# Performance work log

Measured on AMD Instinct MI355X. Metric: run time of the kernel, lower is better.

Reference implementation:

```python
import jax, jax.numpy as jnp
import numpy as np

N_NODES = 50000
N_EDGES = 800000
IN_CH = 128
HIDDEN = 32
HEADS = 4
NEG_SLOPE = 0.2


def segment_softmax(e, seg, num_segments):
    # numerically stable softmax over edges grouped by destination node
    m = jax.ops.segment_max(e, seg, num_segments=num_segments)
    ex = jnp.exp(e - m[seg])
    denom = jax.ops.segment_sum(ex, seg, num_segments=num_segments)
    return ex / denom[seg]


def gat_layer(x, src, dst, W, a_src, a_dst, b, num_nodes, concat):
    H, C = a_src.shape
    h = (x @ W).reshape(num_nodes, H, C)            # (N, H, C)
    alpha_s = jnp.einsum('nhc,hc->nh', h, a_src)    # (N, H)
    alpha_d = jnp.einsum('nhc,hc->nh', h, a_dst)    # (N, H)
    e = jax.nn.leaky_relu(alpha_s[src] + alpha_d[dst], negative_slope=NEG_SLOPE)  # (E, H)
    att = segment_softmax(e, dst, num_nodes)        # (E, H)
    out = jax.ops.segment_sum(h[src] * att[:, :, None], dst, num_segments=num_nodes)  # (N, H, C)
    if concat:
        out = out.reshape(num_nodes, H * C)
    else:
        out = out.mean(axis=1)
    return out + b


def setup_inputs() -> dict:
    key = jax.random.key(0)
    ks = jax.random.split(key, 12)
    s = 0.1
    return {
        'x': jax.random.normal(ks[0], (N_NODES, IN_CH), dtype=jnp.float32),
        'edge_index': jax.random.randint(ks[1], (2, N_EDGES), 0, N_NODES, dtype=jnp.int64),
        'W1': jax.random.normal(ks[2], (IN_CH, HEADS * HIDDEN), dtype=jnp.float32) * s,
        'a_src1': jax.random.normal(ks[3], (HEADS, HIDDEN), dtype=jnp.float32) * s,
        'a_dst1': jax.random.normal(ks[4], (HEADS, HIDDEN), dtype=jnp.float32) * s,
        'b1': jnp.zeros((HEADS * HIDDEN,), dtype=jnp.float32),
        'W2': jax.random.normal(ks[5], (HEADS * HIDDEN, 1 * HIDDEN), dtype=jnp.float32) * s,
        'a_src2': jax.random.normal(ks[6], (1, HIDDEN), dtype=jnp.float32) * s,
        'a_dst2': jax.random.normal(ks[7], (1, HIDDEN), dtype=jnp.float32) * s,
        'b2': jnp.zeros((HIDDEN,), dtype=jnp.float32),
    }


def reference(x, edge_index, W1, a_src1, a_dst1, b1, W2, a_src2, a_dst2, b2):
    n = x.shape[0]
    loops = jnp.arange(n, dtype=edge_index.dtype)
    src = jnp.concatenate([edge_index[0], loops])  # PyG GATConv add_self_loops=True
    dst = jnp.concatenate([edge_index[1], loops])
    h = gat_layer(x, src, dst, W1, a_src1, a_dst1, b1, n, concat=True)
    h = jax.nn.elu(h)  # ELU between layers (dropout=0.0)
    out = gat_layer(h, src, dst, W2, a_src2, a_dst2, b2, n, concat=False)
    return out
```

## Files before the change

### kernel.cpp

```cpp
#include <hip/hip_runtime.h>
#include <cstdint>

#define NEG_SLOPE 0.2f
#define LDA 136
#define HB  128
#define CAP 5120
#define SMEM_BYTES (64 * LDA * 2)

__device__ __forceinline__ float leaky(float v) { return v > 0.f ? v : NEG_SLOPE * v; }
__device__ __forceinline__ float elu(float v) { return v > 0.f ? v : __expf(v) - 1.f; }

typedef _Float16 half2v __attribute__((ext_vector_type(2)));
typedef _Float16 f16x8 __attribute__((ext_vector_type(8)));
typedef float f32x4 __attribute__((ext_vector_type(4)));
union H8 { float4 f4; half2v h[4]; f16x8 v8; };
union H4 { float2 f2; half2v h[2]; };
union HF2 { float2 f2; _Float16 h[4]; };
union HH { f16x8 v; half2v h[4]; };


__device__ __forceinline__ void prep_body(int bid, int G, int tid,
        const float* __restrict__ W1, const float* __restrict__ W2,
        _Float16* __restrict__ W1t, _Float16* __restrict__ W2t) {
    for (int i = bid * 256 + tid; i < 128 * 128; i += G * 256) {
        int c = i >> 7, k = i & 127;
        W1t[i] = (_Float16)W1[k * 128 + c];
    }
    for (int i = bid * 256 + tid; i < 32 * 128; i += G * 256) {
        int c = i >> 7, k = i & 127;
        W2t[i] = (_Float16)W2[k * 32 + c];
    }
}

__device__ __forceinline__ void hist_chunk(int c, int tid, int* lh,
        const int* __restrict__ dstp, int* __restrict__ hist, int E, int NB, int CH) {
    for (int t = tid; t < NB; t += 256) lh[t] = 0;
    __syncthreads();
    int e0 = c * CH, e1 = min(e0 + CH, E);
    int nv = (e1 - e0) & ~3;
    for (int i = e0 + tid * 4; i < e0 + nv; i += 1024) {
        int4 d = *(const int4*)(dstp + i);
        atomicAdd(&lh[d.x >> 8], 1);
        atomicAdd(&lh[d.y >> 8], 1);
        atomicAdd(&lh[d.z >> 8], 1);
        atomicAdd(&lh[d.w >> 8], 1);
    }
    for (int i = e0 + nv + tid; i < e1; i += 256)
        atomicAdd(&lh[dstp[i] >> 8], 1);
    __syncthreads();
    for (int t = tid; t < NB; t += 256) hist[t * HB + c] = lh[t];
}

__device__ __forceinline__ void gemm1_tile(int b, int tid, _Float16* Ah,
        const float* __restrict__ x, const _Float16* __restrict__ W1t,
        const float* __restrict__ a_src, const float* __restrict__ a_dst,
        _Float16* __restrict__ h1h, float* __restrict__ as1, float* __restrict__ ad1,
        int n) {
    int row0 = b * 64;
    const float4* x4 = (const float4*)x;
#pragma unroll
    for (int i = 0; i < 8; ++i) {
        int idx = tid + i * 256;
        int row = idx >> 5, c4 = idx & 31;
        float4 v = make_float4(0.f, 0.f, 0.f, 0.f);
        if (row0 + row < n) v = x4[(size_t)(row0 + row) * 32 + c4];
        HF2 u;
        u.h[0] = (_Float16)v.x; u.h[1] = (_Float16)v.y;
        u.h[2] = (_Float16)v.z; u.h[3] = (_Float16)v.w;
        *(float2*)&Ah[row * LDA + c4 * 4] = u.f2;
    }
    __syncthreads();

    int l = tid & 63, w = tid >> 6;
    int lr = l & 15, lg = l >> 4;
    f16x8 af[4];
#pragma unroll
    for (int kk = 0; kk < 4; ++kk)
        af[kk] = *(const f16x8*)&Ah[(w * 16 + lr) * LDA + kk * 32 + lg * 8];
    f32x4 acc[8];
#pragma unroll
    for (int t = 0; t < 8; ++t) acc[t] = (f32x4)0.f;
#pragma unroll
    for (int t = 0; t < 8; ++t) {
#pragma unroll
        for (int kk = 0; kk < 4; ++kk) {
            f16x8 bf = *(const f16x8*)&W1t[(size_t)(t * 16 + lr) * 128 + kk * 32 + lg * 8];
            acc[t] = __builtin_amdgcn_mfma_f32_16x16x32_f16(af[kk], bf, acc[t], 0, 0, 0);
        }
    }
    __syncthreads();
#pragma unroll
    for (int t = 0; t < 8; ++t)
#pragma unroll
        for (int r = 0; r < 4; ++r)
            Ah[(w * 16 + lg * 4 + r) * LDA + t * 16 + lr] = (_Float16)acc[t][r];
    __syncthreads();
    int row = tid >> 2, q = tid & 3;
    if (row0 + row < n) {
        const float* asv = a_src + q * 32;
        const float* adv = a_dst + q * 32;
        float ps = 0.f, pd = 0.f;
#pragma unroll
        for (int j = 0; j < 4; ++j) {
            f16x8 v = *(const f16x8*)&Ah[row * LDA + q * 32 + j * 8];
            *(f16x8*)&h1h[(size_t)(row0 + row) * 128 + q * 32 + j * 8] = v;
#pragma unroll
            for (int e = 0; e < 8; ++e) {
                float f = (float)v[e];
                ps += f * asv[j * 8 + e];
                pd += f * adv[j * 8 + e];
            }
        }
        as1[(row0 + row) * 4 + q] = ps;
        ad1[(row0 + row) * 4 + q] = pd;
    }
}

__device__ __forceinline__ void pair_chunk(int c, int tid, int* lcur,
        const int* __restrict__ src, const int* __restrict__ dstp,
        const int* __restrict__ hist, int2* __restrict__ pairs,
        int E, int NB, int CH) {
    for (int b = tid; b < NB; b += 256) {
        const int4* row = (const int4*)(hist + b * HB);
        int s = 0;
        int c4 = c >> 2;
#pragma unroll 4
        for (int i = 0; i < c4; ++i) { int4 v = row[i]; s += v.x + v.y + v.z + v.w; }
        for (int i = c4 * 4; i < c; ++i) s += hist[b * HB + i];
        lcur[b] = s;
    }
    __syncthreads();
    int e0 = c * CH, e1 = min(e0 + CH, E);
    int nv = (e1 - e0) & ~3;
    for (int i = e0 + tid * 4; i < e0 + nv; i += 1024) {
        int4 d = *(const int4*)(dstp + i);
        int4 s = *(const int4*)(src + i);
        int b0 = d.x >> 8, b1 = d.y >> 8, b2 = d.z >> 8, b3 = d.w >> 8;
        int r0 = atomicAdd(&lcur[b0], 1);
        int r1 = atomicAdd(&lcur[b1], 1);
        int r2 = atomicAdd(&lcur[b2], 1);
        int r3 = atomicAdd(&lcur[b3], 1);
        if (r0 < CAP) pairs[(size_t)b0 * CAP + r0] = make_int2(s.x, d.x & 255);
        if (r1 < CAP) pairs[(size_t)b1 * CAP + r1] = make_int2(s.y, d.y & 255);
        if (r2 < CAP) pairs[(size_t)b2 * CAP + r2] = make_int2(s.z, d.z & 255);
        if (r3 < CAP) pairs[(size_t)b3 * CAP + r3] = make_int2(s.w, d.w & 255);
    }
    for (int i = e0 + nv + tid; i < e1; i += 256) {
        int d = dstp[i];
        int b = d >> 8;
        int r = atomicAdd(&lcur[b], 1);
        if (r < CAP) pairs[(size_t)b * CAP + r] = make_int2(src[i], d & 255);
    }
}


__global__ __launch_bounds__(256) void prep_hist_kernel(
        const float* __restrict__ W1, const float* __restrict__ W2,
        _Float16* __restrict__ W1t, _Float16* __restrict__ W2t,
        const int* __restrict__ dstp, int* __restrict__ hist, int E, int NB, int CH) {
    __shared__ int lh[256];
    int bid = (int)blockIdx.x;
    if (bid < HB) {
        hist_chunk(bid, threadIdx.x, lh, dstp, hist, E, NB, CH);
        return;
    }
    prep_body(bid - HB, (int)gridDim.x - HB, threadIdx.x, W1, W2, W1t, W2t);
}

__global__ __launch_bounds__(256) void gemm1_pair_kernel(
        const float* __restrict__ x, const _Float16* __restrict__ W1t,
        const float* __restrict__ a_src, const float* __restrict__ a_dst,
        _Float16* __restrict__ h1h, float* __restrict__ as1, float* __restrict__ ad1,
        int n, int gemmBlocks,
        const int* __restrict__ src, const int* __restrict__ dstp,
        const int* __restrict__ hist, int2* __restrict__ pairs, int E, int NB, int CH) {
    __shared__ __align__(16) unsigned char smem[SMEM_BYTES];
    int bid = (int)blockIdx.x;
    if (bid < HB) {
        pair_chunk(bid, threadIdx.x, (int*)smem, src, dstp, hist,
                   pairs, E, NB, CH);
        return;
    }
    gemm1_tile(bid - HB, threadIdx.x, (_Float16*)smem, x, W1t, a_src, a_dst,
               h1h, as1, ad1, n);
}

__global__ __launch_bounds__(256) void csr_kernel(const int2* __restrict__ pairs,
                                                  const int* __restrict__ hist,
                                                  int* __restrict__ rp,
                                                  int* __restrict__ col,
                                                  int E, int N, int NB) {
    __shared__ int lsz[256], lstart[256];
    __shared__ int lnh[256], lnex[256], lncur[256];
    __shared__ int wsum[4], woff[4];
    int b = (int)blockIdx.x, tid = threadIdx.x;
    int lane = tid & 63, wv = tid >> 6;

    {
        int s = 0;
        if (tid < NB) {
            const int4* row = (const int4*)(hist + tid * HB);
#pragma unroll 8
            for (int i = 0; i < HB / 4; ++i) { int4 v = row[i]; s += v.x + v.y + v.z + v.w; }
        }
        lsz[tid] = s;
    }
    __syncthreads();
    int v = lsz[tid];
    int x = v;
#pragma unroll
    for (int o = 1; o < 64; o <<= 1) { int u = __shfl_up(x, o); if (lane >= o) x += u; }
    if (lane == 63) wsum[wv] = x;
    __syncthreads();
    if (tid == 0) { int a = 0; for (int i = 0; i < 4; ++i) { woff[i] = a; a += wsum[i]; } }
    __syncthreads();
    lstart[tid] = x - v + woff[wv];
    __syncthreads();

    if (b >= NB) { if (tid == 0) rp[N] = E; return; }
    int myStart = lstart[b];
    int S = lsz[b]; if (S > CAP) S = CAP;
    const int2* pb = pairs + (size_t)b * CAP;

    lnh[tid] = 0;
    __syncthreads();
    for (int i = tid; i < S; i += 256) atomicAdd(&lnh[pb[i].y], 1);
    __syncthreads();
    int v2 = lnh[tid];
    int x2 = v2;
#pragma unroll
    for (int o = 1; o < 64; o <<= 1) { int u = __shfl_up(x2, o); if (lane >= o) x2 += u; }
    if (lane == 63) wsum[wv] = x2;
    __syncthreads();
    if (tid == 0) { int a = 0; for (int i = 0; i < 4; ++i) { woff[i] = a; a += wsum[i]; } }
    __syncthreads();
    int ex2 = x2 - v2 + woff[wv];
    lnex[tid] = ex2;
    lncur[tid] = 0;
    int node = (b << 8) + tid;
    if (node <= N) rp[node] = myStart + ex2;
    __syncthreads();
    for (int i = tid; i < S; i += 256) {
        int2 p = pb[i];
        int r = atomicAdd(&lncur[p.y], 1);
        col[myStart + lnex[p.y] + r] = p.x;
    }
}

#define W2S 136

__global__ __launch_bounds__(256) void agg1_kernel(const _Float16* __restrict__ h1h,
                                                   const float4* __restrict__ as1,
                                                   const float4* __restrict__ ad1,
                                                   const int* __restrict__ rp,
                                                   const int* __restrict__ col,
                                                   const float* __restrict__ b1,
                                                   const _Float16* __restrict__ W2t,
                                                   const float* __restrict__ a_src2,
                                                   const float* __restrict__ a_dst2,
                                                   _Float16* __restrict__ h2h,
                                                   float* __restrict__ as2,
                                                   float* __restrict__ ad2, int n) {
    __shared__ float4 s_p[4][64];
    __shared__ _Float16 s_row[4][128];
    __shared__ _Float16 sW2[32 * W2S];
    int tid = threadIdx.x;
    for (int e = tid; e < 32 * 16; e += 256) {
        int c = e >> 4, k8 = e & 15;
        *(f16x8*)&sW2[c * W2S + k8 * 8] = *(const f16x8*)&W2t[c * 128 + k8 * 8];
    }
    float a2s = a_src2[tid & 31], a2d = a_dst2[tid & 31];
    __syncthreads();

    int wave = tid >> 6, lane = tid & 63;
    int nid = blockIdx.x * 4 + wave;
    if (nid >= n) return;
    float4* sp = s_p[wave];
    int start = rp[nid], end = rp[nid + 1];
    float4 adn = ad1[nid], asn = as1[nid];
    float4 psf;
    psf.x = __expf(leaky(asn.x + adn.x));
    psf.y = __expf(leaky(asn.y + adn.y));
    psf.z = __expf(leaky(asn.z + adn.z));
    psf.w = __expf(leaky(asn.w + adn.w));
    float4 dsum = make_float4(0.f, 0.f, 0.f, 0.f);
    int g = lane & 15, sub = lane >> 4;
    int head = g >> 2;
    float4 a0 = make_float4(0.f, 0.f, 0.f, 0.f);
    float4 a1 = a0;

    for (int base = start; base < end; base += 64) {
        int i = base + lane;
        int sidx = 0;
        float4 p = make_float4(0.f, 0.f, 0.f, 0.f);
        if (i < end) {
            sidx = col[i];
            float4 a = as1[sidx];
            p.x = __expf(leaky(a.x + adn.x));
            p.y = __expf(leaky(a.y + adn.y));
            p.z = __expf(leaky(a.z + adn.z));
            p.w = __expf(leaky(a.w + adn.w));
            dsum.x += p.x; dsum.y += p.y; dsum.z += p.z; dsum.w += p.w;
        }
        sp[lane] = p;
        int len = min(64, end - base);
        int steps = (len + 3) >> 2;
        for (int s = 0; s < steps; ++s) {
            int j = s * 4 + sub;
            int js = (j < len) ? j : 0;
            int rj = __shfl(sidx, js);
            if (j < len) {
                float pj = ((const float*)&sp[js])[head];
                H8 u = ((const H8*)(h1h + (size_t)rj * 128))[g];
                a0.x += (float)u.h[0].x * pj; a0.y += (float)u.h[0].y * pj;
                a0.z += (float)u.h[1].x * pj; a0.w += (float)u.h[1].y * pj;
                a1.x += (float)u.h[2].x * pj; a1.y += (float)u.h[2].y * pj;
                a1.z += (float)u.h[3].x * pj; a1.w += (float)u.h[3].y * pj;
            }
        }
    }
    if (sub == 0) {
        float pj = (head == 0) ? psf.x : (head == 1) ? psf.y : (head == 2) ? psf.z : psf.w;
        H8 u = ((const H8*)(h1h + (size_t)nid * 128))[g];
        a0.x += (float)u.h[0].x * pj; a0.y += (float)u.h[0].y * pj;
        a0.z += (float)u.h[1].x * pj; a0.w += (float)u.h[1].y * pj;
        a1.x += (float)u.h[2].x * pj; a1.y += (float)u.h[2].y * pj;
        a1.z += (float)u.h[3].x * pj; a1.w += (float)u.h[3].y * pj;
    }
    if (lane == 0) {
        dsum.x += psf.x; dsum.y += psf.y; dsum.z += psf.z; dsum.w += psf.w;
    }
#pragma unroll
    for (int o = 1; o < 64; o <<= 1) {
        dsum.x += __shfl_xor(dsum.x, o); dsum.y += __shfl_xor(dsum.y, o);
        dsum.z += __shfl_xor(dsum.z, o); dsum.w += __shfl_xor(dsum.w, o);
    }
#pragma unroll
    for (int o = 16; o < 64; o <<= 1) {
        a0.x += __shfl_xor(a0.x, o); a0.y += __shfl_xor(a0.y, o);
        a0.z += __shfl_xor(a0.z, o); a0.w += __shfl_xor(a0.w, o);
        a1.x += __shfl_xor(a1.x, o); a1.y += __shfl_xor(a1.y, o);
        a1.z += __shfl_xor(a1.z, o); a1.w += __shfl_xor(a1.w, o);
    }
    if (sub == 0) {
        float den = (head == 0) ? dsum.x : (head == 1) ? dsum.y : (head == 2) ? dsum.z : dsum.w;
        float inv = __builtin_amdgcn_rcpf(den);
        const float4* b4 = (const float4*)b1;
        float4 bb0 = b4[g * 2], bb1 = b4[g * 2 + 1];
        float4 r0 = make_float4(elu(a0.x * inv + bb0.x), elu(a0.y * inv + bb0.y),
                                elu(a0.z * inv + bb0.z), elu(a0.w * inv + bb0.w));
        float4 r1 = make_float4(elu(a1.x * inv + bb1.x), elu(a1.y * inv + bb1.y),
                                elu(a1.z * inv + bb1.z), elu(a1.w * inv + bb1.w));
        H8 o8;
        o8.h[0] = half2v{(_Float16)r0.x, (_Float16)r0.y};
        o8.h[1] = half2v{(_Float16)r0.z, (_Float16)r0.w};
        o8.h[2] = half2v{(_Float16)r1.x, (_Float16)r1.y};
        o8.h[3] = half2v{(_Float16)r1.z, (_Float16)r1.w};
        *(float4*)&s_row[wave][g * 8] = o8.f4;
    }
    int c = lane & 31, half = lane >> 5;
    float acc2 = 0.f;
#pragma unroll
    for (int k8 = 0; k8 < 8; ++k8) {
        HH rv, wvv;
        rv.v  = *(const f16x8*)&s_row[wave][half * 64 + k8 * 8];
        wvv.v = *(const f16x8*)&sW2[c * W2S + half * 64 + k8 * 8];
#if __has_builtin(__builtin_amdgcn_fdot2)
        acc2 = __builtin_amdgcn_fdot2(rv.h[0], wvv.h[0], acc2, false);
        acc2 = __builtin_amdgcn_fdot2(rv.h[1], wvv.h[1], acc2, false);
        acc2 = __builtin_amdgcn_fdot2(rv.h[2], wvv.h[2], acc2, false);
        acc2 = __builtin_amdgcn_fdot2(rv.h[3], wvv.h[3], acc2, false);
#else
#pragma unroll
        for (int e = 0; e < 8; ++e) acc2 += (float)rv.v[e] * (float)wvv.v[e];
#endif
    }
    acc2 += __shfl_xor(acc2, 32);
    float ps = acc2 * a2s, pd = acc2 * a2d;
#pragma unroll
    for (int o = 1; o < 32; o <<= 1) { ps += __shfl_xor(ps, o); pd += __shfl_xor(pd, o); }
    if (lane < 32) h2h[(size_t)nid * 32 + c] = (_Float16)acc2;
    if (lane == 0) { as2[nid] = ps; ad2[nid] = pd; }
}

__global__ __launch_bounds__(256) void agg2_kernel(const _Float16* __restrict__ h2h,
                                                   const float* __restrict__ as2,
                                                   const float* __restrict__ ad2,
                                                   const int* __restrict__ rp,
                                                   const int* __restrict__ col,
                                                   const float* __restrict__ b2,
                                                   float* __restrict__ out, int n) {
    int wave = threadIdx.x >> 6, lane = threadIdx.x & 63;
    int nid = blockIdx.x * 4 + wave;
    if (nid >= n) return;
    int start = rp[nid], end = rp[nid + 1];
    float adn = ad2[nid];
    float psf = __expf(leaky(as2[nid] + adn));
    float dsum = 0.f;
    int g = lane & 7, sub = lane >> 3;
    float4 acc = make_float4(0.f, 0.f, 0.f, 0.f);
    for (int base = start; base < end; base += 64) {
        int i = base + lane;
        int sidx = 0;
        float p = 0.f;
        if (i < end) {
            sidx = col[i];
            p = __expf(leaky(as2[sidx] + adn));
            dsum += p;
        }
        int len = min(64, end - base);
        int steps = (len + 7) >> 3;
        for (int s = 0; s < steps; ++s) {
            int j = s * 8 + sub;
            int js = (j < len) ? j : 0;
            int rj = __shfl(sidx, js);
            float pj = __shfl(p, js);
            if (j < len) {
                H4 u = ((const H4*)(h2h + (size_t)rj * 32))[g];
                acc.x += (float)u.h[0].x * pj; acc.y += (float)u.h[0].y * pj;
                acc.z += (float)u.h[1].x * pj; acc.w += (float)u.h[1].y * pj;
            }
        }
    }
    if (sub == 0) {
        H4 u = ((const H4*)(h2h + (size_t)nid * 32))[g];
        acc.x += (float)u.h[0].x * psf; acc.y += (float)u.h[0].y * psf;
        acc.z += (float)u.h[1].x * psf; acc.w += (float)u.h[1].y * psf;
    }
    if (lane == 0) dsum += psf;
#pragma unroll
    for (int o = 1; o < 64; o <<= 1) dsum += __shfl_xor(dsum, o);
#pragma unroll
    for (int o = 8; o < 64; o <<= 1) {
        acc.x += __shfl_xor(acc.x, o); acc.y += __shfl_xor(acc.y, o);
        acc.z += __shfl_xor(acc.z, o); acc.w += __shfl_xor(acc.w, o);
    }
    if (sub == 0) {
        float inv = __builtin_amdgcn_rcpf(dsum);
        float4 bb = ((const float4*)b2)[g];
        ((float4*)(out + (size_t)nid * 32))[g] =
            make_float4(acc.x * inv + bb.x, acc.y * inv + bb.y,
                        acc.z * inv + bb.z, acc.w * inv + bb.w);
    }
}


extern "C" void kernel_launch(void* const* d_in, const int* in_sizes, int n_in,
                              void* d_out, int out_size, void* d_ws, size_t ws_size,
                              hipStream_t stream) {
    const float* x      = (const float*)d_in[0];
    const int*   ei     = (const int*)d_in[1];
    const float* W1     = (const float*)d_in[2];
    const float* a_src1 = (const float*)d_in[3];
    const float* a_dst1 = (const float*)d_in[4];
    const float* b1     = (const float*)d_in[5];
    const float* W2     = (const float*)d_in[6];
    const float* a_src2 = (const float*)d_in[7];
    const float* a_dst2 = (const float*)d_in[8];
    const float* b2     = (const float*)d_in[9];
    float* out = (float*)d_out;

    const int N = in_sizes[0] / 128;
    const int E = in_sizes[1] / 2;
    const int* src = ei;
    const int* dstp = ei + E;

    uint8_t* w = (uint8_t*)d_ws;
    auto carve = [&](size_t bytes) {
        uint8_t* p = w;
        w += (bytes + 255) & ~(size_t)255;
        return p;
    };
    _Float16* h1h = (_Float16*)carve((size_t)N * 128 * 2);
    _Float16* h2h = (_Float16*)carve((size_t)N * 32 * 2);
    _Float16* W1t = (_Float16*)carve((size_t)128 * 128 * 2);
    _Float16* W2t = (_Float16*)carve((size_t)32 * 128 * 2);
    float* as1 = (float*)carve((size_t)N * 4 * 4);
    float* ad1 = (float*)carve((size_t)N * 4 * 4);
    float* as2 = (float*)carve((size_t)N * 4);
    float* ad2 = (float*)carve((size_t)N * 4);
    int* rp    = (int*)carve((size_t)(N + 1) * 4);
    int* col   = (int*)carve((size_t)E * 4);
    int* hist  = (int*)carve((size_t)256 * HB * 4);

    const int NB = ((N - 1) >> 8) + 1;
    const int KB = (N >> 8) + 1;
    int CH = (E + HB - 1) / HB;
    CH = (CH + 3) & ~3;
    const int gemmBlocks = (N + 63) / 64;
    const int aggGroups = (N + 3) / 4;

    int2* pairs = (int2*)carve((size_t)NB * CAP * 8);

    prep_hist_kernel<<<HB + 80, 256, 0, stream>>>(W1, W2, W1t, W2t, dstp, hist, E, NB, CH);
    gemm1_pair_kernel<<<HB + gemmBlocks, 256, 0, stream>>>(
        x, W1t, a_src1, a_dst1, h1h, as1, ad1, N, gemmBlocks,
        src, dstp, hist, pairs, E, NB, CH);
    csr_kernel<<<KB, 256, 0, stream>>>(pairs, hist, rp, col, E, N, NB);
    agg1_kernel<<<aggGroups, 256, 0, stream>>>(h1h, (const float4*)as1,
                                               (const float4*)ad1, rp, col, b1,
                                               W2t, a_src2, a_dst2, h2h, as2, ad2, N);
    agg2_kernel<<<aggGroups, 256, 0, stream>>>(h2h, as2, ad2, rp, col, b2, out, N);
}
```

Baseline: 215.0 us.

## Co-schedule GEMM1 with CSR build, double histogram chunks, fold softmax denominators

The GEMM1 tiles now run alongside the CSR bucket build in one launch, and edge pairing gets its own kernel. The goal is to overlap the compute-bound GEMM with the latency-bound CSR scatter, not with the pairing pass. The histogram chunk count HB doubles to 256, which gives more parallel blocks in the hist and pair passes but makes the per-bucket row sums in csr_bucket longer. Both aggregation kernels now accumulate the softmax denominator per head inside the gather loop and reduce it with the feature shuffles, which removes a separate full-wave reduction.

```diff
diff --git a/kernel.cpp b/kernel.cpp
--- a/kernel.cpp
+++ b/kernel.cpp
@@ -3,7 +3,7 @@
 
 #define NEG_SLOPE 0.2f
 #define LDA 136
-#define HB  128
+#define HB  256
 #define CAP 5120
 #define SMEM_BYTES (64 * LDA * 2)
 
@@ -49,71 +49,6 @@
         atomicAdd(&lh[dstp[i] >> 8], 1);
     __syncthreads();
     for (int t = tid; t < NB; t += 256) hist[t * HB + c] = lh[t];
-}
-
-__device__ __forceinline__ void gemm1_tile(int b, int tid, _Float16* Ah,
-        const float* __restrict__ x, const _Float16* __restrict__ W1t,
-        const float* __restrict__ a_src, const float* __restrict__ a_dst,
-        _Float16* __restrict__ h1h, float* __restrict__ as1, float* __restrict__ ad1,
-        int n) {
-    int row0 = b * 64;
-    const float4* x4 = (const float4*)x;
-#pragma unroll
-    for (int i = 0; i < 8; ++i) {
-        int idx = tid + i * 256;
-        int row = idx >> 5, c4 = idx & 31;
-        float4 v = make_float4(0.f, 0.f, 0.f, 0.f);
-        if (row0 + row < n) v = x4[(size_t)(row0 + row) * 32 + c4];
-        HF2 u;
-        u.h[0] = (_Float16)v.x; u.h[1] = (_Float16)v.y;
-        u.h[2] = (_Float16)v.z; u.h[3] = (_Float16)v.w;
-        *(float2*)&Ah[row * LDA + c4 * 4] = u.f2;
-    }
-    __syncthreads();
-
-    int l = tid & 63, w = tid >> 6;
-    int lr = l & 15, lg = l >> 4;
-    f16x8 af[4];
-#pragma unroll
-    for (int kk = 0; kk < 4; ++kk)
-        af[kk] = *(const f16x8*)&Ah[(w * 16 + lr) * LDA + kk * 32 + lg * 8];
-    f32x4 acc[8];
-#pragma unroll
-    for (int t = 0; t < 8; ++t) acc[t] = (f32x4)0.f;
-#pragma unroll
-    for (int t = 0; t < 8; ++t) {
-#pragma unroll
-        for (int kk = 0; kk < 4; ++kk) {
-            f16x8 bf = *(const f16x8*)&W1t[(size_t)(t * 16 + lr) * 128 + kk * 32 + lg * 8];
-            acc[t] = __builtin_amdgcn_mfma_f32_16x16x32_f16(af[kk], bf, acc[t], 0, 0, 0);
-        }
-    }
-    __syncthreads();
-#pragma unroll
-    for (int t = 0; t < 8; ++t)
-#pragma unroll
-        for (int r = 0; r < 4; ++r)
-            Ah[(w * 16 + lg * 4 + r) * LDA + t * 16 + lr] = (_Float16)acc[t][r];
-    __syncthreads();
-    int row = tid >> 2, q = tid & 3;
-    if (row0 + row < n) {
-        const float* asv = a_src + q * 32;
-        const float* adv = a_dst + q * 32;
-        float ps = 0.f, pd = 0.f;
-#pragma unroll
-        for (int j = 0; j < 4; ++j) {
-            f16x8 v = *(const f16x8*)&Ah[row * LDA + q * 32 + j * 8];
-            *(f16x8*)&h1h[(size_t)(row0 + row) * 128 + q * 32 + j * 8] = v;
-#pragma unroll
-            for (int e = 0; e < 8; ++e) {
-                float f = (float)v[e];
-                ps += f * asv[j * 8 + e];
-                pd += f * adv[j * 8 + e];
-            }
-        }
-        as1[(row0 + row) * 4 + q] = ps;
-        ad1[(row0 + row) * 4 + q] = pd;
-    }
 }
 
 __device__ __forceinline__ void pair_chunk(int c, int tid, int* lcur,
@@ -153,6 +88,134 @@
     }
 }
 
+__device__ __forceinline__ void gemm1_tile(int b, int tid, _Float16* Ah,
+        const float* __restrict__ x, const _Float16* __restrict__ W1t,
+        const float* __restrict__ a_src, const float* __restrict__ a_dst,
+        _Float16* __restrict__ h1h, float* __restrict__ as1, float* __restrict__ ad1,
+        int n) {
+    int row0 = b * 64;
+    const float4* x4 = (const float4*)x;
+#pragma unroll
+    for (int i = 0; i < 8; ++i) {
+        int idx = tid + i * 256;
+        int row = idx >> 5, c4 = idx & 31;
+        float4 v = make_float4(0.f, 0.f, 0.f, 0.f);
+        if (row0 + row < n) v = x4[(size_t)(row0 + row) * 32 + c4];
+        HF2 u;
+        u.h[0] = (_Float16)v.x; u.h[1] = (_Float16)v.y;
+        u.h[2] = (_Float16)v.z; u.h[3] = (_Float16)v.w;
+        *(float2*)&Ah[row * LDA + c4 * 4] = u.f2;
+    }
+    __syncthreads();
+
+    int l = tid & 63, w = tid >> 6;
+    int lr = l & 15, lg = l >> 4;
+    f16x8 af[4];
+#pragma unroll
+    for (int kk = 0; kk < 4; ++kk)
+        af[kk] = *(const f16x8*)&Ah[(w * 16 + lr) * LDA + kk * 32 + lg * 8];
+    f32x4 acc[8];
+#pragma unroll
+    for (int t = 0; t < 8; ++t) acc[t] = (f32x4)0.f;
+#pragma unroll
+    for (int t = 0; t < 8; ++t) {
+#pragma unroll
+        for (int kk = 0; kk < 4; ++kk) {
+            f16x8 bf = *(const f16x8*)&W1t[(size_t)(t * 16 + lr) * 128 + kk * 32 + lg * 8];
+            acc[t] = __builtin_amdgcn_mfma_f32_16x16x32_f16(af[kk], bf, acc[t], 0, 0, 0);
+        }
+    }
+    __syncthreads();
+#pragma unroll
+    for (int t = 0; t < 8; ++t)
+#pragma unroll
+        for (int r = 0; r < 4; ++r)
+            Ah[(w * 16 + lg * 4 + r) * LDA + t * 16 + lr] = (_Float16)acc[t][r];
+    __syncthreads();
+    int row = tid >> 2, q = tid & 3;
+    if (row0 + row < n) {
+        const float* asv = a_src + q * 32;
+        const float* adv = a_dst + q * 32;
+        float ps = 0.f, pd = 0.f;
+#pragma unroll
+        for (int j = 0; j < 4; ++j) {
+            f16x8 v = *(const f16x8*)&Ah[row * LDA + q * 32 + j * 8];
+            *(f16x8*)&h1h[(size_t)(row0 + row) * 128 + q * 32 + j * 8] = v;
+#pragma unroll
+            for (int e = 0; e < 8; ++e) {
+                float f = (float)v[e];
+                ps += f * asv[j * 8 + e];
+                pd += f * adv[j * 8 + e];
+            }
+        }
+        as1[(row0 + row) * 4 + q] = ps;
+        ad1[(row0 + row) * 4 + q] = pd;
+    }
+}
+
+__device__ __forceinline__ void csr_bucket(int b, int tid, unsigned char* smem,
+        const int2* __restrict__ pairs, const int* __restrict__ hist,
+        int* __restrict__ rp, int* __restrict__ col, int E, int N, int NB) {
+    int* lsz    = (int*)smem;
+    int* lstart = lsz + 256;
+    int* lnh    = lstart + 256;
+    int* lnex   = lnh + 256;
+    int* lncur  = lnex + 256;
+    int* wsum   = lncur + 256;
+    int* woff   = wsum + 4;
+    int lane = tid & 63, wv = tid >> 6;
+
+    {
+        int s = 0;
+        if (tid < NB) {
+            const int4* row = (const int4*)(hist + tid * HB);
+#pragma unroll 8
+            for (int i = 0; i < HB / 4; ++i) { int4 v = row[i]; s += v.x + v.y + v.z + v.w; }
+        }
+        lsz[tid] = s;
+    }
+    __syncthreads();
+    int v = lsz[tid];
+    int x = v;
+#pragma unroll
+    for (int o = 1; o < 64; o <<= 1) { int u = __shfl_up(x, o); if (lane >= o) x += u; }
+    if (lane == 63) wsum[wv] = x;
+    __syncthreads();
+    if (tid == 0) { int a = 0; for (int i = 0; i < 4; ++i) { woff[i] = a; a += wsum[i]; } }
+    __syncthreads();
+    lstart[tid] = x - v + woff[wv];
+    __syncthreads();
+
+    if (b >= NB) { if (tid == 0) rp[N] = E; return; }
+    int myStart = lstart[b];
+    int S = lsz[b]; if (S > CAP) S = CAP;
+    const int2* pb = pairs + (size_t)b * CAP;
+
+    lnh[tid] = 0;
+    __syncthreads();
+    for (int i = tid; i < S; i += 256) atomicAdd(&lnh[pb[i].y], 1);
+    __syncthreads();
+    int v2 = lnh[tid];
+    int x2 = v2;
+#pragma unroll
+    for (int o = 1; o < 64; o <<= 1) { int u = __shfl_up(x2, o); if (lane >= o) x2 += u; }
+    if (lane == 63) wsum[wv] = x2;
+    __syncthreads();
+    if (tid == 0) { int a = 0; for (int i = 0; i < 4; ++i) { woff[i] = a; a += wsum[i]; } }
+    __syncthreads();
+    int ex2 = x2 - v2 + woff[wv];
+    lnex[tid] = ex2;
+    lncur[tid] = 0;
+    int node = (b << 8) + tid;
+    if (node <= N) rp[node] = myStart + ex2;
+    __syncthreads();
+    for (int i = tid; i < S; i += 256) {
+        int2 p = pb[i];
+        int r = atomicAdd(&lncur[p.y], 1);
+        col[myStart + lnex[p.y] + r] = p.x;
+    }
+}
+
 
 __global__ __launch_bounds__(256) void prep_hist_kernel(
         const float* __restrict__ W1, const float* __restrict__ W2,
@@ -167,84 +230,29 @@
     prep_body(bid - HB, (int)gridDim.x - HB, threadIdx.x, W1, W2, W1t, W2t);
 }
 
-__global__ __launch_bounds__(256) void gemm1_pair_kernel(
+__global__ __launch_bounds__(256) void pair_kernel(const int* __restrict__ src,
+                                                   const int* __restrict__ dstp,
+                                                   const int* __restrict__ hist,
+                                                   int2* __restrict__ pairs,
+                                                   int E, int NB, int CH) {
+    __shared__ int lcur[256];
+    pair_chunk(blockIdx.x, threadIdx.x, lcur, src, dstp, hist, pairs, E, NB, CH);
+}
+
+__global__ __launch_bounds__(256) void csr_gemm_kernel(
+        const int2* __restrict__ pairs, const int* __restrict__ hist,
+        int* __restrict__ rp, int* __restrict__ col, int E, int N, int NB, int KB,
         const float* __restrict__ x, const _Float16* __restrict__ W1t,
         const float* __restrict__ a_src, const float* __restrict__ a_dst,
-        _Float16* __restrict__ h1h, float* __restrict__ as1, float* __restrict__ ad1,
-        int n, int gemmBlocks,
-        const int* __restrict__ src, const int* __restrict__ dstp,
-        const int* __restrict__ hist, int2* __restrict__ pairs, int E, int NB, int CH) {
+        _Float16* __restrict__ h1h, float* __restrict__ as1, float* __restrict__ ad1) {
     __shared__ __align__(16) unsigned char smem[SMEM_BYTES];
     int bid = (int)blockIdx.x;
-    if (bid < HB) {
-        pair_chunk(bid, threadIdx.x, (int*)smem, src, dstp, hist,
-                   pairs, E, NB, CH);
+    if (bid < KB) {
+        csr_bucket(bid, threadIdx.x, smem, pairs, hist, rp, col, E, N, NB);
         return;
     }
-    gemm1_tile(bid - HB, threadIdx.x, (_Float16*)smem, x, W1t, a_src, a_dst,
-               h1h, as1, ad1, n);
-}
-
-__global__ __launch_bounds__(256) void csr_kernel(const int2* __restrict__ pairs,
-                                                  const int* __restrict__ hist,
-                                                  int* __restrict__ rp,
-                                                  int* __restrict__ col,
-                                                  int E, int N, int NB) {
-    __shared__ int lsz[256], lstart[256];
-    __shared__ int lnh[256], lnex[256], lncur[256];
-    __shared__ int wsum[4], woff[4];
-    int b = (int)blockIdx.x, tid = threadIdx.x;
-    int lane = tid & 63, wv = tid >> 6;
-
-    {
-        int s = 0;
-        if (tid < NB) {
-            const int4* row = (const int4*)(hist + tid * HB);
-#pragma unroll 8
-            for (int i = 0; i < HB / 4; ++i) { int4 v = row[i]; s += v.x + v.y + v.z + v.w; }
-        }
-        lsz[tid] = s;
-    }
-    __syncthreads();
-    int v = lsz[tid];
-    int x = v;
-#pragma unroll
-    for (int o = 1; o < 64; o <<= 1) { int u = __shfl_up(x, o); if (lane >= o) x += u; }
-    if (lane == 63) wsum[wv] = x;
-    __syncthreads();
-    if (tid == 0) { int a = 0; for (int i = 0; i < 4; ++i) { woff[i] = a; a += wsum[i]; } }
-    __syncthreads();
-    lstart[tid] = x - v + woff[wv];
-    __syncthreads();
-
-    if (b >= NB) { if (tid == 0) rp[N] = E; return; }
-    int myStart = lstart[b];
-    int S = lsz[b]; if (S > CAP) S = CAP;
-    const int2* pb = pairs + (size_t)b * CAP;
-
-    lnh[tid] = 0;
-    __syncthreads();
-    for (int i = tid; i < S; i += 256) atomicAdd(&lnh[pb[i].y], 1);
-    __syncthreads();
-    int v2 = lnh[tid];
-    int x2 = v2;
-#pragma unroll
-    for (int o = 1; o < 64; o <<= 1) { int u = __shfl_up(x2, o); if (lane >= o) x2 += u; }
-    if (lane == 63) wsum[wv] = x2;
-    __syncthreads();
-    if (tid == 0) { int a = 0; for (int i = 0; i < 4; ++i) { woff[i] = a; a += wsum[i]; } }
-    __syncthreads();
-    int ex2 = x2 - v2 + woff[wv];
-    lnex[tid] = ex2;
-    lncur[tid] = 0;
-    int node = (b << 8) + tid;
-    if (node <= N) rp[node] = myStart + ex2;
-    __syncthreads();
-    for (int i = tid; i < S; i += 256) {
-        int2 p = pb[i];
-        int r = atomicAdd(&lncur[p.y], 1);
-        col[myStart + lnex[p.y] + r] = p.x;
-    }
+    gemm1_tile(bid - KB, threadIdx.x, (_Float16*)smem, x, W1t, a_src, a_dst,
+               h1h, as1, ad1, N);
 }
 
 #define W2S 136
@@ -278,14 +286,12 @@
     float4* sp = s_p[wave];
     int start = rp[nid], end = rp[nid + 1];
     float4 adn = ad1[nid], asn = as1[nid];
-    float4 psf;
-    psf.x = __expf(leaky(asn.x + adn.x));
-    psf.y = __expf(leaky(asn.y + adn.y));
-    psf.z = __expf(leaky(asn.z + adn.z));
-    psf.w = __expf(leaky(asn.w + adn.w));
-    float4 dsum = make_float4(0.f, 0.f, 0.f, 0.f);
     int g = lane & 15, sub = lane >> 4;
     int head = g >> 2;
+    float sv = (head == 0) ? asn.x + adn.x : (head == 1) ? asn.y + adn.y
+             : (head == 2) ? asn.z + adn.z : asn.w + adn.w;
+    float psf_h = __expf(leaky(sv));
+    float dnum = 0.f;
     float4 a0 = make_float4(0.f, 0.f, 0.f, 0.f);
     float4 a1 = a0;
 
@@ -300,7 +306,6 @@
             p.y = __expf(leaky(a.y + adn.y));
             p.z = __expf(leaky(a.z + adn.z));
             p.w = __expf(leaky(a.w + adn.w));
-            dsum.x += p.x; dsum.y += p.y; dsum.z += p.z; dsum.w += p.w;
         }
         sp[lane] = p;
         int len = min(64, end - base);
@@ -311,6 +316,7 @@
             int rj = __shfl(sidx, js);
             if (j < len) {
                 float pj = ((const float*)&sp[js])[head];
+                dnum += pj;
                 H8 u = ((const H8*)(h1h + (size_t)rj * 128))[g];
                 a0.x += (float)u.h[0].x * pj; a0.y += (float)u.h[0].y * pj;
                 a0.z += (float)u.h[1].x * pj; a0.w += (float)u.h[1].y * pj;
@@ -320,20 +326,12 @@
         }
     }
     if (sub == 0) {
-        float pj = (head == 0) ? psf.x : (head == 1) ? psf.y : (head == 2) ? psf.z : psf.w;
         H8 u = ((const H8*)(h1h + (size_t)nid * 128))[g];
-        a0.x += (float)u.h[0].x * pj; a0.y += (float)u.h[0].y * pj;
-        a0.z += (float)u.h[1].x * pj; a0.w += (float)u.h[1].y * pj;
-        a1.x += (float)u.h[2].x * pj; a1.y += (float)u.h[2].y * pj;
-        a1.z += (float)u.h[3].x * pj; a1.w += (float)u.h[3].y * pj;
-    }
-    if (lane == 0) {
-        dsum.x += psf.x; dsum.y += psf.y; dsum.z += psf.z; dsum.w += psf.w;
-    }
-#pragma unroll
-    for (int o = 1; o < 64; o <<= 1) {
-        dsum.x += __shfl_xor(dsum.x, o); dsum.y += __shfl_xor(dsum.y, o);
-        dsum.z += __shfl_xor(dsum.z, o); dsum.w += __shfl_xor(dsum.w, o);
+        dnum += psf_h;
+        a0.x += (float)u.h[0].x * psf_h; a0.y += (float)u.h[0].y * psf_h;
+        a0.z += (float)u.h[1].x * psf_h; a0.w += (float)u.h[1].y * psf_h;
+        a1.x += (float)u.h[2].x * psf_h; a1.y += (float)u.h[2].y * psf_h;
+        a1.z += (float)u.h[3].x * psf_h; a1.w += (float)u.h[3].y * psf_h;
     }
 #pragma unroll
     for (int o = 16; o < 64; o <<= 1) {
@@ -341,10 +339,10 @@
         a0.z += __shfl_xor(a0.z, o); a0.w += __shfl_xor(a0.w, o);
         a1.x += __shfl_xor(a1.x, o); a1.y += __shfl_xor(a1.y, o);
         a1.z += __shfl_xor(a1.z, o); a1.w += __shfl_xor(a1.w, o);
+        dnum += __shfl_xor(dnum, o);
     }
     if (sub == 0) {
-        float den = (head == 0) ? dsum.x : (head == 1) ? dsum.y : (head == 2) ? dsum.z : dsum.w;
-        float inv = __builtin_amdgcn_rcpf(den);
+        float inv = __builtin_amdgcn_rcpf(dnum);
         const float4* b4 = (const float4*)b1;
         float4 bb0 = b4[g * 2], bb1 = b4[g * 2 + 1];
         float4 r0 = make_float4(elu(a0.x * inv + bb0.x), elu(a0.y * inv + bb0.y),
@@ -396,8 +394,8 @@
     int start = rp[nid], end = rp[nid + 1];
     float adn = ad2[nid];
     float psf = __expf(leaky(as2[nid] + adn));
-    float dsum = 0.f;
     int g = lane & 7, sub = lane >> 3;
+    float dnum = 0.f;
     float4 acc = make_float4(0.f, 0.f, 0.f, 0.f);
     for (int base = start; base < end; base += 64) {
         int i = base + lane;
@@ -406,7 +404,6 @@
         if (i < end) {
             sidx = col[i];
             p = __expf(leaky(as2[sidx] + adn));
-            dsum += p;
         }
         int len = min(64, end - base);
         int steps = (len + 7) >> 3;
@@ -416,6 +413,7 @@
             int rj = __shfl(sidx, js);
             float pj = __shfl(p, js);
             if (j < len) {
+                dnum += pj;
                 H4 u = ((const H4*)(h2h + (size_t)rj * 32))[g];
                 acc.x += (float)u.h[0].x * pj; acc.y += (float)u.h[0].y * pj;
                 acc.z += (float)u.h[1].x * pj; acc.w += (float)u.h[1].y * pj;
@@ -424,19 +422,18 @@
     }
     if (sub == 0) {
         H4 u = ((const H4*)(h2h + (size_t)nid * 32))[g];
+        dnum += psf;
         acc.x += (float)u.h[0].x * psf; acc.y += (float)u.h[0].y * psf;
         acc.z += (float)u.h[1].x * psf; acc.w += (float)u.h[1].y * psf;
     }
-    if (lane == 0) dsum += psf;
-#pragma unroll
-    for (int o = 1; o < 64; o <<= 1) dsum += __shfl_xor(dsum, o);
 #pragma unroll
     for (int o = 8; o < 64; o <<= 1) {
         acc.x += __shfl_xor(acc.x, o); acc.y += __shfl_xor(acc.y, o);
         acc.z += __shfl_xor(acc.z, o); acc.w += __shfl_xor(acc.w, o);
+        dnum += __shfl_xor(dnum, o);
     }
     if (sub == 0) {
-        float inv = __builtin_amdgcn_rcpf(dsum);
+        float inv = __builtin_amdgcn_rcpf(dnum);
         float4 bb = ((const float4*)b2)[g];
         ((float4*)(out + (size_t)nid * 32))[g] =
             make_float4(acc.x * inv + bb.x, acc.y * inv + bb.y,
@@ -493,10 +490,10 @@
     int2* pairs = (int2*)carve((size_t)NB * CAP * 8);
 
     prep_hist_kernel<<<HB + 80, 256, 0, stream>>>(W1, W2, W1t, W2t, dstp, hist, E, NB, CH);
-    gemm1_pair_kernel<<<HB + gemmBlocks, 256, 0, stream>>>(
-        x, W1t, a_src1, a_dst1, h1h, as1, ad1, N, gemmBlocks,
-        src, dstp, hist, pairs, E, NB, CH);
-    csr_kernel<<<KB, 256, 0, stream>>>(pairs, hist, rp, col, E, N, NB);
+    pair_kernel<<<HB, 256, 0, stream>>>(src, dstp, hist, pairs, E, NB, CH);
+    csr_gemm_kernel<<<KB + gemmBlocks, 256, 0, stream>>>(
+        pairs, hist, rp, col, E, N, NB, KB,
+        x, W1t, a_src1, a_dst1, h1h, as1, ad1);
     agg1_kernel<<<aggGroups, 256, 0, stream>>>(h1h, (const float4*)as1,
                                                (const float4*)ad1, rp, col, b1,
                                                W2t, a_src2, a_dst2, h2h, as2, ad2, N);
```

After: 206.8 us. 1.04x faster.
